# Kernel tuning notes

Measured on AMD Instinct MI355X. Metric: run time of the kernel, lower is better.

Reference implementation:

```python
import jax, jax.numpy as jnp
import numpy as np

B, L, H = 2, 2048, 1024
NH, HD = 16, 64  # n_heads, head_size


def setup_inputs() -> dict:
    key = jax.random.key(0)
    ks = jax.random.split(key, 12)
    scale = 1.0 / np.sqrt(H)
    inp = {
        "hidden_states": jax.random.normal(ks[0], (B, L, H), dtype=jnp.float32),
        "tau": jax.random.uniform(ks[1], (B, 1), dtype=jnp.float32) + 0.5,
        "delta": jax.random.normal(ks[2], (B, L), dtype=jnp.float32) * 0.1,
        "Wq": jax.random.normal(ks[3], (H, H), dtype=jnp.float32) * scale,
        "bq": jnp.zeros((H,), dtype=jnp.float32),
        "Wk": jax.random.normal(ks[4], (H, H), dtype=jnp.float32) * scale,
        "bk": jnp.zeros((H,), dtype=jnp.float32),
        "Wv": jax.random.normal(ks[5], (H, H), dtype=jnp.float32) * scale,
        "bv": jnp.zeros((H,), dtype=jnp.float32),
        "Wo": jax.random.normal(ks[6], (H, H), dtype=jnp.float32) * scale,
        "bo": jnp.zeros((H,), dtype=jnp.float32),
    }
    return inp


def _split_heads(x):
    # [B, L, H] -> [B, NH, L, HD]
    return x.reshape(B, L, NH, HD).transpose(0, 2, 1, 3)


def reference(hidden_states, tau, delta, Wq, bq, Wk, bk, Wv, bv, Wo, bo):
    q = _split_heads(hidden_states @ Wq.T + bq)
    k = _split_heads(hidden_states @ Wk.T + bk)
    v = _split_heads(hidden_states @ Wv.T + bv)
    tau_b = tau[:, :, None, None]          # [B,1,1,1]
    delta_b = delta[:, None, None, :]      # [B,1,1,L]
    scores = jnp.einsum('bhqd,bhkd->bhqk', q, k) * tau_b + delta_b
    scores = scores / np.sqrt(HD)
    attn = jax.nn.softmax(scores, axis=-1)  # dropout = identity (eval mode)
    ctx = jnp.einsum('bhqk,bhkd->bhqd', attn, v)
    ctx = ctx.transpose(0, 2, 1, 3).reshape(B, L, H)
    return ctx @ Wo.T + bo
```

## Files before the change

kernel.cpp:

```cpp
#include <hip/hip_runtime.h>

#define B_ 2
#define L_ 2048
#define H_ 1024
#define NH_ 16
#define HD_ 64

using short8 = __attribute__((__ext_vector_type__(8))) short;
using f32x4 = __attribute__((__ext_vector_type__(4))) float;
using f32x16 = __attribute__((__ext_vector_type__(16))) float;
typedef unsigned short u16;
typedef unsigned int u32;

__device__ __forceinline__ u16 f2bf(float f) {
  union { float f; unsigned u; } x{f};
  unsigned u = x.u;
  u = u + 0x7FFFu + ((u >> 16) & 1u);
  return (u16)(u >> 16);
}

__device__ __forceinline__ void gld16(const void* g, void* l) {
  __builtin_amdgcn_global_load_lds(
      (const __attribute__((address_space(1))) void*)g,
      (__attribute__((address_space(3))) void*)l, 16, 0, 0);
}

#define MFMA16(a, b, c) __builtin_amdgcn_mfma_f32_16x16x32_bf16((a), (b), (c), 0, 0, 0)
#define MFMA32(a, b, c) __builtin_amdgcn_mfma_f32_32x32x16_bf16((a), (b), (c), 0, 0, 0)

__global__ void cast_all(const float* __restrict__ hs, const float* __restrict__ Wq,
                         const float* __restrict__ Wk, const float* __restrict__ Wv,
                         const float* __restrict__ Wo, const float* __restrict__ delta,
                         u16* __restrict__ dst, u16* __restrict__ dscb) {
  const int t = blockIdx.x * 256 + threadIdx.x;
  const int i = t * 4;
  const float* src;
  int off;
  if (i < 4194304) {
    src = hs; off = i;
  } else {
    const int j = i - 4194304;
    const int w = j >> 20;
    off = j & 1048575;
    src = (w == 0) ? Wq : (w == 1) ? Wk : (w == 2) ? Wv : Wo;
  }
  float4 v = *(const float4*)(src + off);
  *(ushort4*)(dst + i) = make_ushort4(f2bf(v.x), f2bf(v.y), f2bf(v.z), f2bf(v.w));
  if (t < 4096) dscb[t] = f2bf(delta[t] * 0.18033688011112042f);
}

__global__ __launch_bounds__(512) void gemm_qkv192(
    const u16* __restrict__ A, const u16* __restrict__ W,
    const float* __restrict__ bq, const float* __restrict__ bk, const float* __restrict__ bv,
    const float* __restrict__ tau,
    u16* __restrict__ qg, u16* __restrict__ kg, u16* __restrict__ vTg) {
  __shared__ u16 As[2][256 * 64];
  __shared__ u16 Bs[2][192 * 64];
  const int tid = threadIdx.x;
  const int lane = tid & 63;
  const int wid = tid >> 6;
  const int wr = wid >> 2;
  const int wc = wid & 3;
  const int orig = blockIdx.y * 16 + blockIdx.x;
  const int wg = (orig & 7) * 32 + (orig >> 3);
  const int m0 = (wg & 15) * 256;
  const int n0 = (wg >> 4) * 192;

  const int srow = tid >> 3;
  const int sg = tid & 7;

#define STAGEQ(slot, t_)                                                                \
  {                                                                                     \
    const int kt64 = (t_) * 64;                                                         \
    _Pragma("unroll") for (int li = 0; li < 4; li++) {                                  \
      const int row = li * 64 + srow;                                                   \
      const int gsrc = sg ^ (row & 7);                                                  \
      gld16(A + (size_t)(m0 + row) * 1024 + kt64 + gsrc * 8,                            \
            (char*)As[slot] + li * 8192 + wid * 1024 + lane * 16);                      \
    }                                                                                   \
    _Pragma("unroll") for (int li = 0; li < 3; li++) {                                  \
      const int row = li * 64 + srow;                                                   \
      const int gsrc = sg ^ (row & 7);                                                  \
      gld16(W + (size_t)(n0 + row) * 1024 + kt64 + gsrc * 8,                            \
            (char*)Bs[slot] + li * 8192 + wid * 1024 + lane * 16);                      \
    }                                                                                   \
  }

  f32x4 acc[8][3] = {};

  STAGEQ(0, 0);
  STAGEQ(1, 1);

  for (int t = 0; t < 16; t++) {
    if (t >= 1 && t + 1 < 16) STAGEQ((t + 1) & 1, t + 1);
    if (t + 1 < 16) {
      asm volatile("s_waitcnt vmcnt(7)" ::: "memory");
    } else {
      asm volatile("s_waitcnt vmcnt(0)" ::: "memory");
    }
    asm volatile("s_barrier" ::: "memory");
    const u16* Ab = As[t & 1];
    const u16* Bb = Bs[t & 1];
    short8 bf[3];
#pragma unroll
    for (int q = 0; q < 4; q++) {
      const int mh = q & 1, ks = q >> 1;
      const int g0 = ks * 4 + (lane >> 4);
      if (mh == 0) {
#pragma unroll
        for (int ni = 0; ni < 3; ni++) {
          const int r = wc * 48 + ni * 16 + (lane & 15);
          bf[ni] = *(const short8*)((const char*)Bb + r * 128 + ((g0 ^ (r & 7)) << 4));
        }
      }
      short8 af[4];
#pragma unroll
      for (int mi = 0; mi < 4; mi++) {
        const int r = wr * 128 + (mh * 4 + mi) * 16 + (lane & 15);
        af[mi] = *(const short8*)((const char*)Ab + r * 128 + ((g0 ^ (r & 7)) << 4));
      }
      __builtin_amdgcn_s_setprio(1);
#pragma unroll
      for (int mi = 0; mi < 4; mi++)
#pragma unroll
        for (int ni = 0; ni < 3; ni++)
          acc[mh * 4 + mi][ni] = MFMA16(af[mi], bf[ni], acc[mh * 4 + mi][ni]);
      __builtin_amdgcn_s_setprio(0);
      asm volatile("s_barrier" ::: "memory");
    }
  }

  const int b_blk = m0 >> 11;
  const float tauv = tau[b_blk] * 0.18033688011112042f;
#pragma unroll
  for (int ni = 0; ni < 3; ni++) {
    const int nbase = n0 + wc * 48 + ni * 16;
    const int which = nbase >> 10;
    const int n = nbase + (lane & 15);
    const int nn = n & 1023;
    const int h = nn >> 6, d = nn & 63;
    const float* bias = which == 0 ? bq : (which == 1 ? bk : bv);
    const float bb = bias[nn];
    const float scl = which == 0 ? tauv : 1.0f;
#pragma unroll
    for (int mi = 0; mi < 8; mi++) {
      const int mb = m0 + wr * 128 + mi * 16 + ((lane >> 4) << 2);
      const int b = mb >> 11;
      const int lq = mb & 2047;
      if (which == 2) {
        ushort4 pk = make_ushort4(f2bf(acc[mi][ni][0] + bb), f2bf(acc[mi][ni][1] + bb),
                                  f2bf(acc[mi][ni][2] + bb), f2bf(acc[mi][ni][3] + bb));
        *(ushort4*)&vTg[((size_t)(b * NH_ + h) * HD_ + d) * L_ + lq] = pk;
      } else {
        u16* dst = which == 0 ? qg : kg;
#pragma unroll
        for (int r = 0; r < 4; r++)
          dst[((size_t)(b * NH_ + h) * L_ + lq + r) * HD_ + d] = f2bf((acc[mi][ni][r] + bb) * scl);
      }
    }
  }
}

__global__ __launch_bounds__(512) void attn(
    const u16* __restrict__ qg, const u16* __restrict__ kg, const u16* __restrict__ vTg,
    const u16* __restrict__ dscb, u16* __restrict__ ctxg) {
  __shared__ u16 lds[3][8192];
  const int tid = threadIdx.x;
  const int lane = tid & 63;
  const int wv = tid >> 6;
  const int lane31 = lane & 31;
  const int hi = lane >> 5;
  const int orig = blockIdx.x;
  const int wgid = (orig & 7) * 32 + (orig >> 3);
  const int bh = wgid >> 3;
  const int qblk = wgid & 7;
  const int b = bh >> 4;
  const int h = bh & 15;
  const int q0 = qblk * 256 + wv * 32;
  const u16* qb = qg + (size_t)bh * L_ * HD_;
  const u16* kb = kg + (size_t)bh * L_ * HD_;
  const u16* vb = vTg + (size_t)bh * HD_ * L_;
  const u16* dbb = dscb + (size_t)b * L_;

  short8 qf[4];
#pragma unroll
  for (int ks = 0; ks < 4; ks++)
    qf[ks] = *(const short8*)&qb[(size_t)(q0 + lane31) * 64 + ks * 16 + hi * 8];

  union U8 { u32 u[4]; short8 s; };
  U8 onesu;
  const u32 ow = (lane31 == 0) ? 0x3F803F80u : 0u;
  onesu.u[0] = ow; onesu.u[1] = ow; onesu.u[2] = ow; onesu.u[3] = ow;
  const short8 onesf = onesu.s;
  U8 onesbu;
  onesbu.u[0] = (hi == 0) ? 0x00003F80u : 0u;
  onesbu.u[1] = 0; onesbu.u[2] = 0; onesbu.u[3] = 0;
  const short8 onesB = onesbu.s;

  f32x16 acc[2] = {};
  f32x16 accl = {};
  float mrun = -__builtin_inff();

#define STAGE(bp_, j0)                                                                    \
  {                                                                                       \
    u16* bp = (bp_);                                                                      \
    {                                                                                     \
      const int kt = wv >> 2, ks = wv & 3;                                                \
      gld16(kb + (size_t)((j0) + kt * 32 + lane31) * 64 + ks * 16 + hi * 8,               \
            bp + wv * 512 + lane * 8);                                                    \
    }                                                                                     \
    {                                                                                     \
      const int kt = wv >> 2, dt = (wv >> 1) & 1, ks2 = wv & 1;                           \
      gld16(vb + (size_t)(dt * 32 + lane31) * L_ + (j0) + kt * 32 + ks2 * 16 + hi * 8,    \
            bp + (8 + wv) * 512 + lane * 8);                                              \
    }                                                                                     \
  }

#define QK64(bp_, j_, sA_, sB_)                                                           \
  {                                                                                       \
    const u16* bp = (bp_);                                                                \
    U8 df0, df1;                                                                          \
    df0.u[0] = (hi == 0) ? (u32)dbb[(j_) + lane31] : 0u;                                  \
    df0.u[1] = 0; df0.u[2] = 0; df0.u[3] = 0;                                             \
    df1.u[0] = (hi == 0) ? (u32)dbb[(j_) + 32 + lane31] : 0u;                             \
    df1.u[1] = 0; df1.u[2] = 0; df1.u[3] = 0;                                             \
    __builtin_amdgcn_s_setprio(1);                                                        \
    sA_ = MFMA32(df0.s, onesB, sA_);                                                      \
    sB_ = MFMA32(df1.s, onesB, sB_);                                                      \
    _Pragma("unroll") for (int ks = 0; ks < 4; ks++) {                                    \
      short8 kf0 = *(const short8*)&bp[(0 * 4 + ks) * 512 + lane * 8];                    \
      short8 kf1 = *(const short8*)&bp[(1 * 4 + ks) * 512 + lane * 8];                    \
      sA_ = MFMA32(kf0, qf[ks], sA_);                                                     \
      sB_ = MFMA32(kf1, qf[ks], sB_);                                                     \
    }                                                                                     \
    __builtin_amdgcn_s_setprio(0);                                                        \
  }

  STAGE(lds[0], 0);
  STAGE(lds[1], 64);
  __syncthreads();

  f32x16 sp0 = {}, sp1 = {};
  QK64(lds[0], 0, sp0, sp1);

  int cur = 0, nxt = 1, fut = 2;
  for (int t = 0; t < 32; t++) {
    const int j0 = t * 64;
    if (t + 2 < 32) STAGE(lds[fut], j0 + 128);
    f32x16 sn0 = {}, sn1 = {};
    if (t + 1 < 32) QK64(lds[nxt], j0 + 64, sn0, sn1);

    float tm[4];
#pragma unroll
    for (int r = 0; r < 4; r++) {
      float a0 = fmaxf(fmaxf(sp0[r], sp0[4 + r]), fmaxf(sp0[8 + r], sp0[12 + r]));
      float a1 = fmaxf(fmaxf(sp1[r], sp1[4 + r]), fmaxf(sp1[8 + r], sp1[12 + r]));
      tm[r] = fmaxf(a0, a1);
    }
    float pmax = fmaxf(fmaxf(tm[0], tm[1]), fmaxf(tm[2], tm[3]));
    pmax = fmaxf(pmax, __shfl_xor(pmax, 32));
    if (!__all(pmax - mrun <= 11.5f)) {
      float mnew = fmaxf(mrun, pmax);
      float al = __builtin_amdgcn_exp2f(mrun - mnew);
      mrun = mnew;
      accl[0] *= al;
#pragma unroll
      for (int dt = 0; dt < 2; dt++)
#pragma unroll
        for (int r = 0; r < 16; r++) acc[dt][r] *= al;
    }

    const u16* bp = lds[cur];
#pragma unroll
    for (int r = 0; r < 16; r++) sp0[r] = __builtin_amdgcn_exp2f(sp0[r] - mrun);
    u32 pk0[8];
#pragma unroll
    for (int i = 0; i < 8; i++)
      asm("v_cvt_pk_bf16_f32 %0, %1, %2" : "=v"(pk0[i]) : "v"(sp0[2 * i]), "v"(sp0[2 * i + 1]));
    asm volatile("v_permlane32_swap_b32 %0, %1" : "+v"(pk0[0]), "+v"(pk0[2]));
    asm volatile("v_permlane32_swap_b32 %0, %1" : "+v"(pk0[1]), "+v"(pk0[3]));
    asm volatile("v_permlane32_swap_b32 %0, %1" : "+v"(pk0[4]), "+v"(pk0[6]));
    asm volatile("v_permlane32_swap_b32 %0, %1" : "+v"(pk0[5]), "+v"(pk0[7]));
    __builtin_amdgcn_s_setprio(1);
#pragma unroll
    for (int ks2 = 0; ks2 < 2; ks2++) {
      U8 pf;
      pf.u[0] = pk0[ks2 * 4 + 0]; pf.u[1] = pk0[ks2 * 4 + 1];
      pf.u[2] = pk0[ks2 * 4 + 2]; pf.u[3] = pk0[ks2 * 4 + 3];
#pragma unroll
      for (int dt = 0; dt < 2; dt++) {
        short8 vf = *(const short8*)&bp[(8 + 0 * 4 + dt * 2 + ks2) * 512 + lane * 8];
        acc[dt] = MFMA32(vf, pf.s, acc[dt]);
      }
      accl = MFMA32(onesf, pf.s, accl);
    }
    __builtin_amdgcn_s_setprio(0);
#pragma unroll
    for (int r = 0; r < 16; r++) sp1[r] = __builtin_amdgcn_exp2f(sp1[r] - mrun);
    u32 pk1[8];
#pragma unroll
    for (int i = 0; i < 8; i++)
      asm("v_cvt_pk_bf16_f32 %0, %1, %2" : "=v"(pk1[i]) : "v"(sp1[2 * i]), "v"(sp1[2 * i + 1]));
    asm volatile("v_permlane32_swap_b32 %0, %1" : "+v"(pk1[0]), "+v"(pk1[2]));
    asm volatile("v_permlane32_swap_b32 %0, %1" : "+v"(pk1[1]), "+v"(pk1[3]));
    asm volatile("v_permlane32_swap_b32 %0, %1" : "+v"(pk1[4]), "+v"(pk1[6]));
    asm volatile("v_permlane32_swap_b32 %0, %1" : "+v"(pk1[5]), "+v"(pk1[7]));
    __builtin_amdgcn_s_setprio(1);
#pragma unroll
    for (int ks2 = 0; ks2 < 2; ks2++) {
      U8 pf;
      pf.u[0] = pk1[ks2 * 4 + 0]; pf.u[1] = pk1[ks2 * 4 + 1];
      pf.u[2] = pk1[ks2 * 4 + 2]; pf.u[3] = pk1[ks2 * 4 + 3];
#pragma unroll
      for (int dt = 0; dt < 2; dt++) {
        short8 vf = *(const short8*)&bp[(8 + 1 * 4 + dt * 2 + ks2) * 512 + lane * 8];
        acc[dt] = MFMA32(vf, pf.s, acc[dt]);
      }
      accl = MFMA32(onesf, pf.s, accl);
    }
    __builtin_amdgcn_s_setprio(0);
    __syncthreads();
    sp0 = sn0; sp1 = sn1;
    const int tmp = cur; cur = nxt; nxt = fut; fut = tmp;
  }

  u16* tw = (u16*)lds + wv * 2048;
  const float l0 = accl[0];
  const float l1 = __shfl_xor(l0, 32);
  const float inv = 1.0f / (hi ? l1 : l0);
#pragma unroll
  for (int dt = 0; dt < 2; dt++)
#pragma unroll
    for (int g = 0; g < 4; g++) {
      ushort4 w4 = make_ushort4(f2bf(acc[dt][g * 4 + 0] * inv), f2bf(acc[dt][g * 4 + 1] * inv),
                                f2bf(acc[dt][g * 4 + 2] * inv), f2bf(acc[dt][g * 4 + 3] * inv));
      const int d0 = dt * 32 + g * 8 + hi * 4;
      const int byte = (lane31 * 128 + d0 * 2) ^ ((lane31 & 15) << 3);
      *(ushort4*)((char*)tw + byte) = w4;
    }
  asm volatile("s_waitcnt lgkmcnt(0)" ::: "memory");
  const size_t obase = ((size_t)b * L_ + q0) * 1024 + h * 64;
#pragma unroll
  for (int i = 0; i < 16; i++) {
    const int qr = 2 * i + hi;
    const int byte = (qr * 128 + lane31 * 4) ^ ((qr & 15) << 3);
    const u32 val = *(const u32*)((const char*)tw + byte);
    *(u32*)&ctxg[obase + (size_t)qr * 1024 + lane31 * 2] = val;
  }
}

__global__ __launch_bounds__(256) void gemm_out128(
    const u16* __restrict__ A, const u16* __restrict__ W,
    const float* __restrict__ bo, float* __restrict__ out) {
  __shared__ u16 As[2][128 * 64];
  __shared__ u16 Bs[2][128 * 64];
  const int tid = threadIdx.x;
  const int lane = tid & 63;
  const int wid = tid >> 6;
  const int wr = wid >> 1;
  const int wc = wid & 1;
  const int orig = blockIdx.y * 8 + blockIdx.x;
  const int wg = (orig & 7) * 32 + (orig >> 3);
  const int m0 = (wg & 31) * 128;
  const int n0 = (wg >> 5) * 128;

  const int srow = tid >> 3;
  const int sg = tid & 7;

#define STAGEO(slot, t_)                                                                \
  {                                                                                     \
    const int kt64 = (t_) * 64;                                                         \
    _Pragma("unroll") for (int li = 0; li < 4; li++) {                                  \
      const int row = li * 32 + srow;                                                   \
      const int gsrc = sg ^ (row & 7);                                                  \
      gld16(A + (size_t)(m0 + row) * 1024 + kt64 + gsrc * 8,                            \
            (char*)As[slot] + li * 4096 + wid * 1024 + lane * 16);                      \
      gld16(W + (size_t)(n0 + row) * 1024 + kt64 + gsrc * 8,                            \
            (char*)Bs[slot] + li * 4096 + wid * 1024 + lane * 16);                      \
    }                                                                                   \
  }

  f32x4 acc[4][4] = {};

  STAGEO(0, 0);
  STAGEO(1, 1);

  for (int t = 0; t < 16; t++) {
    if (t >= 1 && t + 1 < 16) STAGEO((t + 1) & 1, t + 1);
    if (t + 1 < 16) {
      asm volatile("s_waitcnt vmcnt(8)" ::: "memory");
    } else {
      asm volatile("s_waitcnt vmcnt(0)" ::: "memory");
    }
    asm volatile("s_barrier" ::: "memory");
    const u16* Ab = As[t & 1];
    const u16* Bb = Bs[t & 1];
    short8 bf[4];
#pragma unroll
    for (int q = 0; q < 4; q++) {
      const int mh = q & 1, ks = q >> 1;
      const int g0 = ks * 4 + (lane >> 4);
      if (mh == 0) {
#pragma unroll
        for (int ni = 0; ni < 4; ni++) {
          const int r = wc * 64 + ni * 16 + (lane & 15);
          bf[ni] = *(const short8*)((const char*)Bb + r * 128 + ((g0 ^ (r & 7)) << 4));
        }
      }
      short8 af[2];
#pragma unroll
      for (int mi = 0; mi < 2; mi++) {
        const int r = wr * 64 + (mh * 2 + mi) * 16 + (lane & 15);
        af[mi] = *(const short8*)((const char*)Ab + r * 128 + ((g0 ^ (r & 7)) << 4));
      }
      __builtin_amdgcn_s_setprio(1);
#pragma unroll
      for (int mi = 0; mi < 2; mi++)
#pragma unroll
        for (int ni = 0; ni < 4; ni++)
          acc[mh * 2 + mi][ni] = MFMA16(af[mi], bf[ni], acc[mh * 2 + mi][ni]);
      __builtin_amdgcn_s_setprio(0);
      asm volatile("s_barrier" ::: "memory");
    }
  }

#pragma unroll
  for (int ni = 0; ni < 4; ni++) {
    const int n = n0 + wc * 64 + ni * 16 + (lane & 15);
    const float bb = bo[n];
#pragma unroll
    for (int mi = 0; mi < 4; mi++) {
      const int mb = m0 + wr * 64 + mi * 16 + ((lane >> 4) << 2);
#pragma unroll
      for (int r = 0; r < 4; r++)
        out[(size_t)(mb + r) * 1024 + n] = acc[mi][ni][r] + bb;
    }
  }
}

extern "C" void kernel_launch(void* const* d_in, const int* in_sizes, int n_in,
                              void* d_out, int out_size, void* d_ws, size_t ws_size,
                              hipStream_t stream) {
  const float* hs = (const float*)d_in[0];
  const float* tau = (const float*)d_in[1];
  const float* delta = (const float*)d_in[2];
  const float* Wq = (const float*)d_in[3];
  const float* bq = (const float*)d_in[4];
  const float* Wk = (const float*)d_in[5];
  const float* bk = (const float*)d_in[6];
  const float* Wv = (const float*)d_in[7];
  const float* bv = (const float*)d_in[8];
  const float* Wo = (const float*)d_in[9];
  const float* bo = (const float*)d_in[10];
  float* out = (float*)d_out;

  u16* ws = (u16*)d_ws;
  u16* hsb  = ws;
  u16* wqkv = ws + 4194304;
  u16* wob  = ws + 7340032;
  u16* qg   = ws + 8388608;
  u16* kg   = ws + 12582912;
  u16* vTg  = ws + 16777216;
  u16* ctxg = ws + 20971520;
  u16* dscb = ws + 25165824;

  cast_all<<<8192, 256, 0, stream>>>(hs, Wq, Wk, Wv, Wo, delta, ws, dscb);

  gemm_qkv192<<<dim3(16, 16), 512, 0, stream>>>(hsb, wqkv, bq, bk, bv, tau, qg, kg, vTg);
  attn<<<256, 512, 0, stream>>>(qg, kg, vTg, dscb, ctxg);
  gemm_out128<<<dim3(8, 32), 256, 0, stream>>>(ctxg, wob, bo, out);
}
```

Measured before the change: 132.9 us.

## Use 128-key double-buffered tiles and drop software-pipelined QK prefetch in attention

The attention loop now processes 128 keys per iteration with two LDS buffers instead of 64 keys with a triple buffer. It also removes the software pipelining that computed the next tile's QK scores while the current tile's softmax and PV ran. The aim is to halve the number of barriers and online-softmax max/rescale steps and to simplify scheduling. In exchange it loses QK/softmax overlap across iterations, keeps four score fragments live at once (more register pressure), and uses more LDS per block.

Result: no change. 134.5 us (+1.1%).

```diff
diff --git a/kernel.cpp b/kernel.cpp
--- a/kernel.cpp
+++ b/kernel.cpp
@@ -164,7 +164,7 @@
 __global__ __launch_bounds__(512) void attn(
     const u16* __restrict__ qg, const u16* __restrict__ kg, const u16* __restrict__ vTg,
     const u16* __restrict__ dscb, u16* __restrict__ ctxg) {
-  __shared__ u16 lds[3][8192];
+  __shared__ u16 lds[2][16384];
   const int tid = threadIdx.x;
   const int lane = tid & 63;
   const int wv = tid >> 6;
@@ -201,61 +201,56 @@
   f32x16 accl = {};
   float mrun = -__builtin_inff();
 
-#define STAGE(bp_, j0)                                                                    \
+#define STAGE(bp_, j0_)                                                                   \
   {                                                                                       \
     u16* bp = (bp_);                                                                      \
-    {                                                                                     \
-      const int kt = wv >> 2, ks = wv & 3;                                                \
-      gld16(kb + (size_t)((j0) + kt * 32 + lane31) * 64 + ks * 16 + hi * 8,               \
-            bp + wv * 512 + lane * 8);                                                    \
+    _Pragma("unroll") for (int s = 0; s < 2; s++) {                                       \
+      const int i = 2 * wv + s;                                                           \
+      const int kt = i >> 2, ks = i & 3;                                                  \
+      gld16(kb + (size_t)((j0_) + kt * 32 + lane31) * 64 + ks * 16 + hi * 8,              \
+            bp + i * 512 + lane * 8);                                                     \
     }                                                                                     \
-    {                                                                                     \
-      const int kt = wv >> 2, dt = (wv >> 1) & 1, ks2 = wv & 1;                           \
-      gld16(vb + (size_t)(dt * 32 + lane31) * L_ + (j0) + kt * 32 + ks2 * 16 + hi * 8,    \
-            bp + (8 + wv) * 512 + lane * 8);                                              \
+    _Pragma("unroll") for (int s = 0; s < 2; s++) {                                       \
+      const int i = 2 * wv + s;                                                           \
+      const int kt = i >> 2, dt = (i >> 1) & 1, ks2 = i & 1;                              \
+      gld16(vb + (size_t)(dt * 32 + lane31) * L_ + (j0_) + kt * 32 + ks2 * 16 + hi * 8,   \
+            bp + (16 + i) * 512 + lane * 8);                                              \
     }                                                                                     \
   }
 
-#define QK64(bp_, j_, sA_, sB_)                                                           \
-  {                                                                                       \
-    const u16* bp = (bp_);                                                                \
-    U8 df0, df1;                                                                          \
-    df0.u[0] = (hi == 0) ? (u32)dbb[(j_) + lane31] : 0u;                                  \
-    df0.u[1] = 0; df0.u[2] = 0; df0.u[3] = 0;                                             \
-    df1.u[0] = (hi == 0) ? (u32)dbb[(j_) + 32 + lane31] : 0u;                             \
-    df1.u[1] = 0; df1.u[2] = 0; df1.u[3] = 0;                                             \
-    __builtin_amdgcn_s_setprio(1);                                                        \
-    sA_ = MFMA32(df0.s, onesB, sA_);                                                      \
-    sB_ = MFMA32(df1.s, onesB, sB_);                                                      \
-    _Pragma("unroll") for (int ks = 0; ks < 4; ks++) {                                    \
-      short8 kf0 = *(const short8*)&bp[(0 * 4 + ks) * 512 + lane * 8];                    \
-      short8 kf1 = *(const short8*)&bp[(1 * 4 + ks) * 512 + lane * 8];                    \
-      sA_ = MFMA32(kf0, qf[ks], sA_);                                                     \
-      sB_ = MFMA32(kf1, qf[ks], sB_);                                                     \
-    }                                                                                     \
-    __builtin_amdgcn_s_setprio(0);                                                        \
-  }
-
   STAGE(lds[0], 0);
-  STAGE(lds[1], 64);
   __syncthreads();
 
-  f32x16 sp0 = {}, sp1 = {};
-  QK64(lds[0], 0, sp0, sp1);
-
-  int cur = 0, nxt = 1, fut = 2;
-  for (int t = 0; t < 32; t++) {
-    const int j0 = t * 64;
-    if (t + 2 < 32) STAGE(lds[fut], j0 + 128);
-    f32x16 sn0 = {}, sn1 = {};
-    if (t + 1 < 32) QK64(lds[nxt], j0 + 64, sn0, sn1);
+  for (int t = 0; t < 16; t++) {
+    const int j0 = t * 128;
+    if (t + 1 < 16) STAGE(lds[(t + 1) & 1], j0 + 128);
+    const u16* bp = lds[t & 1];
+
+    f32x16 sp[4];
+    __builtin_amdgcn_s_setprio(1);
+#pragma unroll
+    for (int kt = 0; kt < 4; kt++) {
+      U8 df;
+      df.u[0] = (hi == 0) ? (u32)dbb[j0 + kt * 32 + lane31] : 0u;
+      df.u[1] = 0; df.u[2] = 0; df.u[3] = 0;
+      f32x16 s = MFMA32(df.s, onesB, f32x16{});
+#pragma unroll
+      for (int ks = 0; ks < 4; ks++) {
+        short8 kf = *(const short8*)&bp[(kt * 4 + ks) * 512 + lane * 8];
+        s = MFMA32(kf, qf[ks], s);
+      }
+      sp[kt] = s;
+    }
+    __builtin_amdgcn_s_setprio(0);
 
     float tm[4];
 #pragma unroll
     for (int r = 0; r < 4; r++) {
-      float a0 = fmaxf(fmaxf(sp0[r], sp0[4 + r]), fmaxf(sp0[8 + r], sp0[12 + r]));
-      float a1 = fmaxf(fmaxf(sp1[r], sp1[4 + r]), fmaxf(sp1[8 + r], sp1[12 + r]));
-      tm[r] = fmaxf(a0, a1);
+      float a0 = fmaxf(fmaxf(sp[0][r], sp[0][4 + r]), fmaxf(sp[0][8 + r], sp[0][12 + r]));
+      float a1 = fmaxf(fmaxf(sp[1][r], sp[1][4 + r]), fmaxf(sp[1][8 + r], sp[1][12 + r]));
+      float a2 = fmaxf(fmaxf(sp[2][r], sp[2][4 + r]), fmaxf(sp[2][8 + r], sp[2][12 + r]));
+      float a3 = fmaxf(fmaxf(sp[3][r], sp[3][4 + r]), fmaxf(sp[3][8 + r], sp[3][12 + r]));
+      tm[r] = fmaxf(fmaxf(a0, a1), fmaxf(a2, a3));
     }
     float pmax = fmaxf(fmaxf(tm[0], tm[1]), fmaxf(tm[2], tm[3]));
     pmax = fmaxf(pmax, __shfl_xor(pmax, 32));
@@ -270,58 +265,34 @@
         for (int r = 0; r < 16; r++) acc[dt][r] *= al;
     }
 
-    const u16* bp = lds[cur];
-#pragma unroll
-    for (int r = 0; r < 16; r++) sp0[r] = __builtin_amdgcn_exp2f(sp0[r] - mrun);
-    u32 pk0[8];
-#pragma unroll
-    for (int i = 0; i < 8; i++)
-      asm("v_cvt_pk_bf16_f32 %0, %1, %2" : "=v"(pk0[i]) : "v"(sp0[2 * i]), "v"(sp0[2 * i + 1]));
-    asm volatile("v_permlane32_swap_b32 %0, %1" : "+v"(pk0[0]), "+v"(pk0[2]));
-    asm volatile("v_permlane32_swap_b32 %0, %1" : "+v"(pk0[1]), "+v"(pk0[3]));
-    asm volatile("v_permlane32_swap_b32 %0, %1" : "+v"(pk0[4]), "+v"(pk0[6]));
-    asm volatile("v_permlane32_swap_b32 %0, %1" : "+v"(pk0[5]), "+v"(pk0[7]));
-    __builtin_amdgcn_s_setprio(1);
-#pragma unroll
-    for (int ks2 = 0; ks2 < 2; ks2++) {
-      U8 pf;
-      pf.u[0] = pk0[ks2 * 4 + 0]; pf.u[1] = pk0[ks2 * 4 + 1];
-      pf.u[2] = pk0[ks2 * 4 + 2]; pf.u[3] = pk0[ks2 * 4 + 3];
-#pragma unroll
-      for (int dt = 0; dt < 2; dt++) {
-        short8 vf = *(const short8*)&bp[(8 + 0 * 4 + dt * 2 + ks2) * 512 + lane * 8];
-        acc[dt] = MFMA32(vf, pf.s, acc[dt]);
-      }
-      accl = MFMA32(onesf, pf.s, accl);
-    }
-    __builtin_amdgcn_s_setprio(0);
-#pragma unroll
-    for (int r = 0; r < 16; r++) sp1[r] = __builtin_amdgcn_exp2f(sp1[r] - mrun);
-    u32 pk1[8];
-#pragma unroll
-    for (int i = 0; i < 8; i++)
-      asm("v_cvt_pk_bf16_f32 %0, %1, %2" : "=v"(pk1[i]) : "v"(sp1[2 * i]), "v"(sp1[2 * i + 1]));
-    asm volatile("v_permlane32_swap_b32 %0, %1" : "+v"(pk1[0]), "+v"(pk1[2]));
-    asm volatile("v_permlane32_swap_b32 %0, %1" : "+v"(pk1[1]), "+v"(pk1[3]));
-    asm volatile("v_permlane32_swap_b32 %0, %1" : "+v"(pk1[4]), "+v"(pk1[6]));
-    asm volatile("v_permlane32_swap_b32 %0, %1" : "+v"(pk1[5]), "+v"(pk1[7]));
-    __builtin_amdgcn_s_setprio(1);
-#pragma unroll
-    for (int ks2 = 0; ks2 < 2; ks2++) {
-      U8 pf;
-      pf.u[0] = pk1[ks2 * 4 + 0]; pf.u[1] = pk1[ks2 * 4 + 1];
-      pf.u[2] = pk1[ks2 * 4 + 2]; pf.u[3] = pk1[ks2 * 4 + 3];
-#pragma unroll
-      for (int dt = 0; dt < 2; dt++) {
-        short8 vf = *(const short8*)&bp[(8 + 1 * 4 + dt * 2 + ks2) * 512 + lane * 8];
-        acc[dt] = MFMA32(vf, pf.s, acc[dt]);
-      }
-      accl = MFMA32(onesf, pf.s, accl);
-    }
-    __builtin_amdgcn_s_setprio(0);
+#pragma unroll
+    for (int kt = 0; kt < 4; kt++) {
+#pragma unroll
+      for (int r = 0; r < 16; r++) sp[kt][r] = __builtin_amdgcn_exp2f(sp[kt][r] - mrun);
+      u32 pk[8];
+#pragma unroll
+      for (int i = 0; i < 8; i++)
+        asm("v_cvt_pk_bf16_f32 %0, %1, %2" : "=v"(pk[i]) : "v"(sp[kt][2 * i]), "v"(sp[kt][2 * i + 1]));
+      asm volatile("v_permlane32_swap_b32 %0, %1" : "+v"(pk[0]), "+v"(pk[2]));
+      asm volatile("v_permlane32_swap_b32 %0, %1" : "+v"(pk[1]), "+v"(pk[3]));
+      asm volatile("v_permlane32_swap_b32 %0, %1" : "+v"(pk[4]), "+v"(pk[6]));
+      asm volatile("v_permlane32_swap_b32 %0, %1" : "+v"(pk[5]), "+v"(pk[7]));
+      __builtin_amdgcn_s_setprio(1);
+#pragma unroll
+      for (int ks2 = 0; ks2 < 2; ks2++) {
+        U8 pf;
+        pf.u[0] = pk[ks2 * 4 + 0]; pf.u[1] = pk[ks2 * 4 + 1];
+        pf.u[2] = pk[ks2 * 4 + 2]; pf.u[3] = pk[ks2 * 4 + 3];
+#pragma unroll
+        for (int dt = 0; dt < 2; dt++) {
+          short8 vf = *(const short8*)&bp[(16 + kt * 4 + dt * 2 + ks2) * 512 + lane * 8];
+          acc[dt] = MFMA32(vf, pf.s, acc[dt]);
+        }
+        accl = MFMA32(onesf, pf.s, accl);
+      }
+      __builtin_amdgcn_s_setprio(0);
+    }
     __syncthreads();
-    sp0 = sn0; sp1 = sn1;
-    const int tmp = cur; cur = nxt; nxt = fut; fut = tmp;
   }
 
   u16* tw = (u16*)lds + wv * 2048;
```
